# Performance work log

Hardware: AMD Instinct MI355X
Metric: run time of the kernel (lower is better)

## Reference

```python
import jax, jax.numpy as jnp
import numpy as np

R = 256        # reservoir_size
M = 256        # samples
S = 512        # steps
D = 2          # n_features (dims)
B = 16         # bits_per_feature
LUT_LEN = 18   # 2**18 LUT entries per node; >= max possible state index
OUT = 32       # output_size


def _first_primes(n):
    lim = 2000  # p_256 = 1619 < 2000
    is_p = np.ones(lim, dtype=bool)
    is_p[:2] = False
    for i in range(2, int(lim ** 0.5) + 1):
        if is_p[i]:
            is_p[i * i::i] = False
    return np.nonzero(is_p)[0][:n].astype(np.int32)


def setup_inputs() -> dict:
    key = jax.random.key(0)
    k = jax.random.split(key, 6)
    x = jax.random.randint(k[0], (M, S, D, B), 0, 2).astype(bool)
    lut = jax.random.randint(k[1], (R, 2 ** LUT_LEN), 0, 2).astype(jnp.int32)
    init_res = jax.random.randint(k[2], (R,), 0, 2).astype(bool)
    W = jax.random.randint(k[3], (R, R), 0, 2).astype(bool)
    primes = jnp.asarray(_first_primes(R))  # first R primes, like primes[:reservoir_size]
    input_nodes = jax.random.permutation(k[4], R)[: D * B]  # randperm(R)[:b*d]
    readout_w = jax.random.normal(k[5], (OUT, R), jnp.float32) * (1.0 / np.sqrt(R))
    readout_b = jnp.zeros((OUT,), jnp.float32)
    return dict(x=x, lut=lut, init_res=init_res, W=W, primes=primes,
                input_nodes=input_nodes, readout_w=readout_w, readout_b=readout_b)


def reference(x, lut, init_res, W, primes, input_nodes, readout_w, readout_b):
    m, s, d, b = x.shape
    r = init_res.shape[0]
    xs = x.reshape(m, s, d * b).transpose(1, 0, 2)  # [s, m, nb] time-major for scan
    Wi = W.astype(jnp.int32)                        # [R, R]
    node_idx = jnp.arange(r)                        # [R]

    def step(res, xt):
        # 1. write encoded input bits into the reservoir (scatter)
        res = res.at[:, input_nodes].set(xt)                    # [m, R] bool
        # 2. state_idx[n] = sum_k res[k] * primes[k] * W[n, k]  (primes-weighted masked sum)
        v = res.astype(jnp.int32) * primes                      # [m, R]
        state_idx = v @ Wi.T                                    # [m, R] int32
        # 3. per-node LUT gather -> next boolean state
        res = lut[node_idx[None, :], state_idx].astype(bool)    # [m, R]
        return res, None

    res0 = jnp.broadcast_to(init_res, (m, r))  # every sample starts from initial_reservoir
    res_final, _ = jax.lax.scan(step, res0, xs)
    # readout on final reservoir state
    return res_final.astype(jnp.float32) @ readout_w.T + readout_b  # [m, OUT]
```

## Files before the change

kernel.cpp:

```cpp
#include <hip/hip_runtime.h>
#include <hip/hip_fp16.h>

#define RES 256
#define MS 256
#define ST 512
#define NB 32
#define LUTLEN 262144
#define LUTW 8192
#define NOUT 32
#define NBLK 256

typedef __attribute__((ext_vector_type(8))) _Float16 half8;
typedef __attribute__((ext_vector_type(4))) float f32x4;

__device__ __forceinline__ void publish_barrier() {
    asm volatile("s_waitcnt lgkmcnt(0)" ::: "memory");
    __builtin_amdgcn_s_barrier();
}

__global__ __launch_bounds__(256) void lut_offsets_kernel(const int* __restrict__ W,
                                                          const int* __restrict__ primes,
                                                          int* __restrict__ off) {
    __shared__ int s[RES];
    const int n = threadIdx.x;
    int maxsum = 0;
    for (int k = 0; k < RES; ++k)
        maxsum += (W[n * RES + k] != 0) ? primes[k] : 0;
    int nw = (maxsum >> 5) + 1;
    s[n] = nw;
    __syncthreads();
    for (int d = 1; d < RES; d <<= 1) {
        int v = (n >= d) ? s[n - d] : 0;
        __syncthreads();
        s[n] += v;
        __syncthreads();
    }
    off[n] = s[n] - nw;
    if (n == RES - 1) off[RES] = s[n];
}

__global__ __launch_bounds__(512) void pack_lut2_kernel(const int* __restrict__ lut,
                                                        const int* __restrict__ off,
                                                        unsigned* __restrict__ lutp) {
    const int n = blockIdx.x;
    const int o = off[n];
    const int nw = off[n + 1] - o;
    const int* src = lut + (size_t)n * LUTLEN;
    for (int w = threadIdx.x; w < nw; w += blockDim.x) {
        const int4* p = (const int4*)(src + (size_t)w * 32);
        unsigned word = 0u;
#pragma unroll
        for (int c = 0; c < 8; ++c) {
            const int4 v = p[c];
            word |= (v.x != 0 ? 1u : 0u) << (4 * c + 0);
            word |= (v.y != 0 ? 1u : 0u) << (4 * c + 1);
            word |= (v.z != 0 ? 1u : 0u) << (4 * c + 2);
            word |= (v.w != 0 ? 1u : 0u) << (4 * c + 3);
        }
        lutp[o + w] = word;
    }
}

__global__ __launch_bounds__(256) void pack_x_kernel(const int* __restrict__ x,
                                                     unsigned* __restrict__ xp) {
    const int total = MS * ST;
    int w = blockIdx.x * blockDim.x + threadIdx.x;
    const int stride = gridDim.x * blockDim.x;
    for (; w < total; w += stride) {
        const int4* p = (const int4*)(x + (size_t)w * 32);
        unsigned word = 0u;
#pragma unroll
        for (int c = 0; c < 8; ++c) {
            const int4 v = p[c];
            word |= (v.x != 0 ? 1u : 0u) << (4 * c + 0);
            word |= (v.y != 0 ? 1u : 0u) << (4 * c + 1);
            word |= (v.z != 0 ? 1u : 0u) << (4 * c + 2);
            word |= (v.w != 0 ? 1u : 0u) << (4 * c + 3);
        }
        const int m = w >> 9;
        const int t = w & (ST - 1);
        xp[t * MS + m] = word;
    }
}

template<bool LP, bool XP>
__global__ __launch_bounds__(256, 1) void reservoir_kernel(
    const int* __restrict__ xraw,
    const unsigned* __restrict__ xp,
    const int* __restrict__ lutraw,
    const unsigned* __restrict__ lutp,
    const int* __restrict__ off,
    const int* __restrict__ init_res,
    const int* __restrict__ W,
    const int* __restrict__ primes,
    const int* __restrict__ input_nodes,
    const float* __restrict__ rw,
    const float* __restrict__ rb,
    float* __restrict__ out)
{
    __shared__ __align__(16) _Float16 vArow[2][264];
    __shared__ unsigned xw_lds[ST];

    const int tid = threadIdx.x;
    const int lane = tid & 63;
    const int wid = tid >> 6;
    const int g = lane >> 4;
    const int r = lane & 15;
    const int m0 = blockIdx.x;

    const int nn = wid * 64 + lane;

    const _Float16 pz = (_Float16)(float)primes[nn];
    const _Float16 z  = (_Float16)0.0f;

    const unsigned* lpn = LP ? (lutp + off[nn]) : nullptr;
    int jn = -1;
    for (int j = 0; j < NB; ++j)
        if (input_nodes[j] == nn) jn = j;

    half8 B[4][8];
#pragma unroll
    for (int tau = 0; tau < 4; ++tau) {
        const int nc = wid * 64 + tau * 16 + r;
#pragma unroll
        for (int kc = 0; kc < 8; ++kc) {
            const int kb = kc * 32 + g * 8;
            const int4* wp = (const int4*)(W + nc * RES + kb);
            const int4 wa = wp[0], wb = wp[1];
            half8 b;
            b[0] = wa.x != 0 ? (_Float16)1.0f : z;  b[1] = wa.y != 0 ? (_Float16)1.0f : z;
            b[2] = wa.z != 0 ? (_Float16)1.0f : z;  b[3] = wa.w != 0 ? (_Float16)1.0f : z;
            b[4] = wb.x != 0 ? (_Float16)1.0f : z;  b[5] = wb.y != 0 ? (_Float16)1.0f : z;
            b[6] = wb.z != 0 ? (_Float16)1.0f : z;  b[7] = wb.w != 0 ? (_Float16)1.0f : z;
            B[tau][kc] = b;
        }
    }

    if (XP) {
        xw_lds[tid] = xp[tid * MS + m0];
        xw_lds[tid + 256] = xp[(tid + 256) * MS + m0];
    }

    {
        int b;
        if (XP) {
            const unsigned x0 = xp[m0];
            b = (jn >= 0) ? (int)((x0 >> jn) & 1u) : (init_res[nn] != 0);
        } else {
            b = (jn >= 0) ? (xraw[(m0 * ST) * NB + jn] != 0) : (init_res[nn] != 0);
        }
        vArow[0][nn] = b ? pz : z;
    }
    __syncthreads();

    auto STEP = [&](int cur, int nxt, int t) {
        unsigned xa = 0u;
        if (XP) xa = xw_lds[(t + 1) & (ST - 1)];
        half8 A[8];
#pragma unroll
        for (int kc = 0; kc < 8; ++kc)
            A[kc] = *(const half8*)&vArow[cur][kc * 32 + g * 8];
        f32x4 ca[4], cb[4];
#pragma unroll
        for (int tau = 0; tau < 4; ++tau) { ca[tau] = {0.f,0.f,0.f,0.f}; cb[tau] = {0.f,0.f,0.f,0.f}; }
#pragma unroll
        for (int kc = 0; kc < 8; kc += 2) {
#pragma unroll
            for (int tau = 0; tau < 4; ++tau) {
                ca[tau] = __builtin_amdgcn_mfma_f32_16x16x32_f16(A[kc],   B[tau][kc],   ca[tau], 0, 0, 0);
                cb[tau] = __builtin_amdgcn_mfma_f32_16x16x32_f16(A[kc+1], B[tau][kc+1], cb[tau], 0, 0, 0);
            }
        }
        float f0 = ca[0][0] + cb[0][0];
        float f1 = ca[1][0] + cb[1][0];
        float f2 = ca[2][0] + cb[2][0];
        float f3 = ca[3][0] + cb[3][0];
        float f = (g == 0) ? f0 : (g == 1) ? f1 : (g == 2) ? f2 : f3;
        const unsigned i = (unsigned)f;
        int b;
        if (LP) {
            const unsigned w = lpn[i >> 5];
            b = (int)((w >> (i & 31u)) & 1u);
        } else {
            b = (lutraw[(size_t)nn * LUTLEN + i] != 0);
        }
        if (t != ST - 1 && jn >= 0) {
            b = XP ? (int)((xa >> jn) & 1u)
                   : (xraw[(m0 * ST + t + 1) * NB + jn] != 0);
        }
        vArow[nxt][nn] = b ? pz : z;
        publish_barrier();
    };

#pragma unroll 1
    for (int tt = 0; tt < ST; tt += 2) {
        STEP(0, 1, tt);
        STEP(1, 0, tt + 1);
    }

    if (tid < NOUT) {
        const int o = tid;
        float acc = rb[o];
        for (int n = 0; n < RES; ++n) {
            if (vArow[0][n] != z) acc += rw[o * RES + n];
        }
        out[m0 * NOUT + o] = acc;
    }
}

extern "C" void kernel_launch(void* const* d_in, const int* in_sizes, int n_in,
                              void* d_out, int out_size, void* d_ws, size_t ws_size,
                              hipStream_t stream) {
    const int* x           = (const int*)d_in[0];
    const int* lut         = (const int*)d_in[1];
    const int* init_res    = (const int*)d_in[2];
    const int* W           = (const int*)d_in[3];
    const int* primes      = (const int*)d_in[4];
    const int* input_nodes = (const int*)d_in[5];
    const float* rw        = (const float*)d_in[6];
    const float* rb        = (const float*)d_in[7];
    float* out = (float*)d_out;

    const size_t lutp_bytes = (size_t)RES * LUTW * sizeof(unsigned);
    const size_t xp_bytes   = (size_t)ST * MS * sizeof(unsigned);
    const size_t off_bytes  = (RES + 1) * sizeof(int);

    unsigned* lutp = nullptr;
    unsigned* xp = nullptr;
    int* off = nullptr;
    bool use_lp = false, use_xp = false;
    unsigned char* ws = (unsigned char*)d_ws;
    if (ws_size >= lutp_bytes + xp_bytes + 256 + off_bytes) {
        lutp = (unsigned*)ws;
        xp = (unsigned*)(ws + lutp_bytes);
        off = (int*)(ws + lutp_bytes + xp_bytes);
        use_lp = use_xp = true;
    } else if (ws_size >= xp_bytes) {
        xp = (unsigned*)ws;
        use_xp = true;
    }

    if (use_lp) {
        hipLaunchKernelGGL(lut_offsets_kernel, dim3(1), dim3(256), 0, stream, W, primes, off);
        hipLaunchKernelGGL(pack_lut2_kernel, dim3(RES), dim3(512), 0, stream, lut, off, lutp);
    }
    if (use_xp) hipLaunchKernelGGL(pack_x_kernel, dim3(512), dim3(256), 0, stream, x, xp);

    if (use_lp)
        hipLaunchKernelGGL((reservoir_kernel<true, true>), dim3(NBLK), dim3(256), 0, stream,
                           x, xp, lut, lutp, off, init_res, W, primes, input_nodes, rw, rb, out);
    else if (use_xp)
        hipLaunchKernelGGL((reservoir_kernel<false, true>), dim3(NBLK), dim3(256), 0, stream,
                           x, xp, lut, lutp, off, init_res, W, primes, input_nodes, rw, rb, out);
    else
        hipLaunchKernelGGL((reservoir_kernel<false, false>), dim3(NBLK), dim3(256), 0, stream,
                           x, xp, lut, lutp, off, init_res, W, primes, input_nodes, rw, rb, out);
}
```

Baseline: 428.8 us.

## Spread reservoir step across 16 waves with one 16-node tile each

Each block grows from 4 to 16 wavefronts, and each wave now computes one 16-column MFMA tile (8 MFMAs) instead of four tiles (32 MFMAs). Only the g==0 lanes do the LUT lookup and the write to the shared state row. The goal is to shorten the serial per-step dependency chain by spreading the matvec across more waves. In exchange, each per-step barrier now synchronises 16 waves, three quarters of the lanes sit idle during the gather, and every wave reads the full A row from LDS.

```diff
diff --git a/kernel.cpp b/kernel.cpp
--- a/kernel.cpp
+++ b/kernel.cpp
@@ -84,7 +84,7 @@
 }
 
 template<bool LP, bool XP>
-__global__ __launch_bounds__(256, 1) void reservoir_kernel(
+__global__ __launch_bounds__(1024, 1) void reservoir_kernel(
     const int* __restrict__ xraw,
     const unsigned* __restrict__ xp,
     const int* __restrict__ lutraw,
@@ -108,7 +108,8 @@
     const int r = lane & 15;
     const int m0 = blockIdx.x;
 
-    const int nn = wid * 64 + lane;
+    const int nn = wid * 16 + r;
+    const bool own = (g == 0);
 
     const _Float16 pz = (_Float16)(float)primes[nn];
     const _Float16 z  = (_Float16)0.0f;
@@ -118,30 +119,23 @@
     for (int j = 0; j < NB; ++j)
         if (input_nodes[j] == nn) jn = j;
 
-    half8 B[4][8];
-#pragma unroll
-    for (int tau = 0; tau < 4; ++tau) {
-        const int nc = wid * 64 + tau * 16 + r;
-#pragma unroll
-        for (int kc = 0; kc < 8; ++kc) {
-            const int kb = kc * 32 + g * 8;
-            const int4* wp = (const int4*)(W + nc * RES + kb);
-            const int4 wa = wp[0], wb = wp[1];
-            half8 b;
-            b[0] = wa.x != 0 ? (_Float16)1.0f : z;  b[1] = wa.y != 0 ? (_Float16)1.0f : z;
-            b[2] = wa.z != 0 ? (_Float16)1.0f : z;  b[3] = wa.w != 0 ? (_Float16)1.0f : z;
-            b[4] = wb.x != 0 ? (_Float16)1.0f : z;  b[5] = wb.y != 0 ? (_Float16)1.0f : z;
-            b[6] = wb.z != 0 ? (_Float16)1.0f : z;  b[7] = wb.w != 0 ? (_Float16)1.0f : z;
-            B[tau][kc] = b;
-        }
-    }
-
-    if (XP) {
-        xw_lds[tid] = xp[tid * MS + m0];
-        xw_lds[tid + 256] = xp[(tid + 256) * MS + m0];
-    }
-
-    {
+    half8 B[8];
+#pragma unroll
+    for (int kc = 0; kc < 8; ++kc) {
+        const int kb = kc * 32 + g * 8;
+        const int4* wp = (const int4*)(W + nn * RES + kb);
+        const int4 wa = wp[0], wb = wp[1];
+        half8 b;
+        b[0] = wa.x != 0 ? (_Float16)1.0f : z;  b[1] = wa.y != 0 ? (_Float16)1.0f : z;
+        b[2] = wa.z != 0 ? (_Float16)1.0f : z;  b[3] = wa.w != 0 ? (_Float16)1.0f : z;
+        b[4] = wb.x != 0 ? (_Float16)1.0f : z;  b[5] = wb.y != 0 ? (_Float16)1.0f : z;
+        b[6] = wb.z != 0 ? (_Float16)1.0f : z;  b[7] = wb.w != 0 ? (_Float16)1.0f : z;
+        B[kc] = b;
+    }
+
+    if (XP && tid < ST) xw_lds[tid] = xp[tid * MS + m0];
+
+    if (own) {
         int b;
         if (XP) {
             const unsigned x0 = xp[m0];
@@ -160,35 +154,33 @@
 #pragma unroll
         for (int kc = 0; kc < 8; ++kc)
             A[kc] = *(const half8*)&vArow[cur][kc * 32 + g * 8];
-        f32x4 ca[4], cb[4];
-#pragma unroll
-        for (int tau = 0; tau < 4; ++tau) { ca[tau] = {0.f,0.f,0.f,0.f}; cb[tau] = {0.f,0.f,0.f,0.f}; }
-#pragma unroll
-        for (int kc = 0; kc < 8; kc += 2) {
-#pragma unroll
-            for (int tau = 0; tau < 4; ++tau) {
-                ca[tau] = __builtin_amdgcn_mfma_f32_16x16x32_f16(A[kc],   B[tau][kc],   ca[tau], 0, 0, 0);
-                cb[tau] = __builtin_amdgcn_mfma_f32_16x16x32_f16(A[kc+1], B[tau][kc+1], cb[tau], 0, 0, 0);
+        f32x4 c0 = {0.f,0.f,0.f,0.f}, c1 = {0.f,0.f,0.f,0.f};
+        f32x4 c2 = {0.f,0.f,0.f,0.f}, c3 = {0.f,0.f,0.f,0.f};
+        c0 = __builtin_amdgcn_mfma_f32_16x16x32_f16(A[0], B[0], c0, 0, 0, 0);
+        c1 = __builtin_amdgcn_mfma_f32_16x16x32_f16(A[1], B[1], c1, 0, 0, 0);
+        c2 = __builtin_amdgcn_mfma_f32_16x16x32_f16(A[2], B[2], c2, 0, 0, 0);
+        c3 = __builtin_amdgcn_mfma_f32_16x16x32_f16(A[3], B[3], c3, 0, 0, 0);
+        c0 = __builtin_amdgcn_mfma_f32_16x16x32_f16(A[4], B[4], c0, 0, 0, 0);
+        c1 = __builtin_amdgcn_mfma_f32_16x16x32_f16(A[5], B[5], c1, 0, 0, 0);
+        c2 = __builtin_amdgcn_mfma_f32_16x16x32_f16(A[6], B[6], c2, 0, 0, 0);
+        c3 = __builtin_amdgcn_mfma_f32_16x16x32_f16(A[7], B[7], c3, 0, 0, 0);
+
+        if (own) {
+            const float f = (c0[0] + c1[0]) + (c2[0] + c3[0]);
+            const unsigned i = (unsigned)f;
+            int b;
+            if (LP) {
+                const unsigned w = lpn[i >> 5];
+                b = (int)((w >> (i & 31u)) & 1u);
+            } else {
+                b = (lutraw[(size_t)nn * LUTLEN + i] != 0);
             }
-        }
-        float f0 = ca[0][0] + cb[0][0];
-        float f1 = ca[1][0] + cb[1][0];
-        float f2 = ca[2][0] + cb[2][0];
-        float f3 = ca[3][0] + cb[3][0];
-        float f = (g == 0) ? f0 : (g == 1) ? f1 : (g == 2) ? f2 : f3;
-        const unsigned i = (unsigned)f;
-        int b;
-        if (LP) {
-            const unsigned w = lpn[i >> 5];
-            b = (int)((w >> (i & 31u)) & 1u);
-        } else {
-            b = (lutraw[(size_t)nn * LUTLEN + i] != 0);
-        }
-        if (t != ST - 1 && jn >= 0) {
-            b = XP ? (int)((xa >> jn) & 1u)
-                   : (xraw[(m0 * ST + t + 1) * NB + jn] != 0);
-        }
-        vArow[nxt][nn] = b ? pz : z;
+            if (t != ST - 1 && jn >= 0) {
+                b = XP ? (int)((xa >> jn) & 1u)
+                       : (xraw[(m0 * ST + t + 1) * NB + jn] != 0);
+            }
+            vArow[nxt][nn] = b ? pz : z;
+        }
         publish_barrier();
     };
 
@@ -247,12 +239,12 @@
     if (use_xp) hipLaunchKernelGGL(pack_x_kernel, dim3(512), dim3(256), 0, stream, x, xp);
 
     if (use_lp)
-        hipLaunchKernelGGL((reservoir_kernel<true, true>), dim3(NBLK), dim3(256), 0, stream,
+        hipLaunchKernelGGL((reservoir_kernel<true, true>), dim3(NBLK), dim3(1024), 0, stream,
                            x, xp, lut, lutp, off, init_res, W, primes, input_nodes, rw, rb, out);
     else if (use_xp)
-        hipLaunchKernelGGL((reservoir_kernel<false, true>), dim3(NBLK), dim3(256), 0, stream,
+        hipLaunchKernelGGL((reservoir_kernel<false, true>), dim3(NBLK), dim3(1024), 0, stream,
                            x, xp, lut, lutp, off, init_res, W, primes, input_nodes, rw, rb, out);
     else
-        hipLaunchKernelGGL((reservoir_kernel<false, false>), dim3(NBLK), dim3(256), 0, stream,
+        hipLaunchKernelGGL((reservoir_kernel<false, false>), dim3(NBLK), dim3(1024), 0, stream,
                            x, xp, lut, lutp, off, init_res, W, primes, input_nodes, rw, rb, out);
 }
```

Result: faster. 390.0 us (-9.0%).
